# Optimization experiments

Measured on AMD Instinct MI355X. Metric: run time of the kernel, lower is better.

The kernel has to match this reference:

```python
import jax, jax.numpy as jnp
import numpy as np

HEADS = 8
DIM_HEAD = 32
EPS = 1e-5


def _rel_index(h, w):
    # matches Attention._generate_relative_index (static, computed on host)
    coords = np.stack(np.meshgrid(np.arange(h), np.arange(w), indexing='ij')).reshape(2, -1)
    rel = coords[:, :, None] - coords[:, None, :]  # [2, n, n]
    rel[0] += h - 1
    rel[1] += w - 1
    rel[0] *= 2 * w - 1
    idx = rel.sum(0).reshape(-1)
    # torch.clamp(relative_index, 0, max_index) -- indices are already in range here
    return jnp.asarray(np.clip(idx, 0, (2 * h - 1) * (2 * w - 1) - 1))


def _layernorm(x, g, b):
    m = jnp.mean(x, axis=-1, keepdims=True)
    v = jnp.var(x, axis=-1, keepdims=True)
    return (x - m) * jax.lax.rsqrt(v + EPS) * g + b


def setup_inputs() -> dict:
    key = jax.random.key(0)
    ks = jax.random.split(key, 6)
    B, C, H, W = 64, 384, 16, 16
    inner = HEADS * DIM_HEAD  # 256
    hid = 4 * C               # 1536
    def nrm(k, shape, s=0.02):
        return jax.random.normal(k, shape, jnp.float32) * s
    return {
        'x': jax.random.normal(ks[0], (B, C, H, W), jnp.float32),
        'ln1_g': jnp.ones((C,), jnp.float32),
        'ln1_b': jnp.zeros((C,), jnp.float32),
        'w_qkv': nrm(ks[1], (C, 3 * inner)),
        'bias_table': nrm(ks[2], ((2 * H - 1) * (2 * W - 1), HEADS)),
        'w_out': nrm(ks[3], (inner, C)),
        'b_out': jnp.zeros((C,), jnp.float32),
        'ln2_g': jnp.ones((C,), jnp.float32),
        'ln2_b': jnp.zeros((C,), jnp.float32),
        'w_ff1': nrm(ks[4], (C, hid)),
        'b_ff1': jnp.zeros((hid,), jnp.float32),
        'w_ff2': nrm(ks[5], (hid, C)),
        'b_ff2': jnp.zeros((C,), jnp.float32),
    }


def reference(x, ln1_g, ln1_b, w_qkv, bias_table, w_out, b_out,
              ln2_g, ln2_b, w_ff1, b_ff1, w_ff2, b_ff2):
    B, C, H, W = x.shape
    n = H * W
    t = x.reshape(B, C, n).transpose(0, 2, 1)  # [B, n, C]

    # --- attention branch (PreNorm(LayerNorm) -> Attention) ---
    a = _layernorm(t, ln1_g, ln1_b)
    qkv = a @ w_qkv  # [B, n, 3*inner]
    q, k, v = jnp.split(qkv, 3, axis=-1)
    def split_heads(z):
        return z.reshape(B, n, HEADS, DIM_HEAD).transpose(0, 2, 1, 3)  # [B, h, n, d]
    q, k, v = split_heads(q), split_heads(k), split_heads(v)
    dots = jnp.einsum('bhid,bhjd->bhij', q, k) * (DIM_HEAD ** -0.5)
    idx = _rel_index(H, W)  # [n*n]
    rel_bias = bias_table[idx].reshape(n, n, HEADS).transpose(2, 0, 1)[None]  # [1, h, n, n]
    attn = jax.nn.softmax(dots + rel_bias, axis=-1)
    o = jnp.einsum('bhij,bhjd->bhid', attn, v)
    o = o.transpose(0, 2, 1, 3).reshape(B, n, HEADS * DIM_HEAD)
    attn_out = o @ w_out + b_out  # to_out Linear (dropout=0)

    # --- feedforward branch (PreNorm(LayerNorm) -> FFN) ---
    f = _layernorm(t, ln2_g, ln2_b)
    f = jax.nn.gelu(f @ w_ff1 + b_ff1, approximate=False) @ w_ff2 + b_ff2

    y = t + attn_out + f  # x_adjusted + attn_out + ff_out
    return y.transpose(0, 2, 1).reshape(B, C, H, W)
```

## Files before the change

kernel.cpp:

```cpp
#include <hip/hip_runtime.h>

typedef __bf16 bf16;
typedef __bf16 bf16x8 __attribute__((ext_vector_type(8)));
typedef float f32x4 __attribute__((ext_vector_type(4)));

__device__ __forceinline__ void gll16(const void* g, void* l) {
    __builtin_amdgcn_global_load_lds((const __attribute__((address_space(1))) void*)g,
                                     (__attribute__((address_space(3))) void*)l, 16, 0, 0);
}

#define WBAR(N) asm volatile("s_waitcnt vmcnt(" #N ")\n\ts_barrier" ::: "memory")

__device__ __forceinline__ float gelu_f(float v) {
    float x2 = v * v;
    float sn = v * fmaf(-0.0713540072f, x2, -1.5957691216f);
    float e  = __expf(sn);
    return v * __builtin_amdgcn_rcpf(1.0f + e);
}

__launch_bounds__(256)
__global__ void prep_kernel(const float* __restrict__ wqkv, const float* __restrict__ wout,
                            const float* __restrict__ wff1, const float* __restrict__ wff2,
                            bf16* __restrict__ wqkvT, bf16* __restrict__ woutT,
                            bf16* __restrict__ wff1T, bf16* __restrict__ wff2T,
                            const float* __restrict__ x,
                            const float* __restrict__ g1, const float* __restrict__ b1,
                            const float* __restrict__ g2, const float* __restrict__ b2,
                            bf16* __restrict__ a, bf16* __restrict__ f) {
    __shared__ __align__(16) float smem[12672 + 512 + 64];
    const int tid = threadIdx.x;
    int g = blockIdx.x;
    if (g < 1536) {
        float (*tl)[33] = (float (*)[33])smem;
        const float* in; bf16* out; int R, Cc, bx, by;
        if (g < 288)       { in = wqkv; out = wqkvT; R = 384;  Cc = 768;  bx = g % 24; by = g / 24; }
        else if (g < 384)  { g -= 288; in = wout; out = woutT; R = 256;  Cc = 384;  bx = g % 12; by = g / 12; }
        else if (g < 960)  { g -= 384; in = wff1; out = wff1T; R = 384;  Cc = 1536; bx = g % 48; by = g / 48; }
        else               { g -= 960; in = wff2; out = wff2T; R = 1536; Cc = 384;  bx = g % 12; by = g / 12; }
        const int c0 = bx * 32, r0 = by * 32;
        const int cl = tid & 31, r8 = tid >> 5;
#pragma unroll
        for (int k = 0; k < 4; k++) {
            int r = k * 8 + r8;
            tl[r][cl] = in[(size_t)(r0 + r) * Cc + c0 + cl];
        }
        __syncthreads();
#pragma unroll
        for (int k = 0; k < 4; k++) {
            int cc = k * 8 + r8;
            out[(size_t)(c0 + cc) * R + r0 + cl] = (bf16)tl[cl][cc];
        }
        return;
    }
    g -= 1536;
    float (*tile)[33] = (float (*)[33])smem;
    float (*S)[32]  = (float (*)[32])(smem + 12672);
    float (*SS)[32] = (float (*)[32])(smem + 12928);
    float* Mn = smem + 13184;
    float* Rs = smem + 13216;
    const int bb = g >> 3;
    const int i0 = (g & 7) * 32;
    {
        const int i_l = tid & 31, c_l = tid >> 5;
        const size_t base = (size_t)bb * 384 * 256 + i0 + i_l;
#pragma unroll 6
        for (int c = c_l; c < 384; c += 8)
            tile[c][i_l] = x[base + (size_t)c * 256];
    }
    __syncthreads();
    {
        const int i_s = tid & 31, p = tid >> 5;
        float s = 0.f, ss = 0.f;
#pragma unroll 6
        for (int j = 0; j < 48; j++) {
            float v = tile[p * 48 + j][i_s];
            s += v; ss += v * v;
        }
        S[p][i_s] = s; SS[p][i_s] = ss;
    }
    __syncthreads();
    if (tid < 32) {
        float t1 = 0.f, t2 = 0.f;
#pragma unroll
        for (int p = 0; p < 8; p++) { t1 += S[p][tid]; t2 += SS[p][tid]; }
        float mean = t1 * (1.0f / 384.0f);
        float var  = t2 * (1.0f / 384.0f) - mean * mean;
        Mn[tid] = mean;
        Rs[tid] = rsqrtf(var + 1e-5f);
    }
    __syncthreads();
    const int lane = tid & 63, w = tid >> 6;
#pragma unroll
    for (int rr = 0; rr < 8; rr++) {
        const int i = w * 8 + rr;
        const float mean = Mn[i], rstd = Rs[i];
        const size_t orow = ((size_t)bb * 256 + i0 + i) * 384;
#pragma unroll
        for (int pass = 0; pass < 6; pass++) {
            const int c = pass * 64 + lane;
            float nh = (tile[c][i] - mean) * rstd;
            a[orow + c] = (bf16)(nh * g1[c] + b1[c]);
            f[orow + c] = (bf16)(nh * g2[c] + b2[c]);
        }
    }
}

#define STAGEW(buf, kb)                                                     \
    {                                                                       \
        bf16* sA = lds + (buf) * 12288;                                     \
        bf16* sB = sA + 4096;                                               \
        gll16(Abase + (size_t)rS * K + (kb) + ksw, sA + tid * 8);           \
        gll16(Abase + (size_t)(rS + 64) * K + (kb) + ksw, sA + (tid + 256) * 8); \
        gll16(Bbase + (size_t)rS * K + (kb) + ksw, sB + tid * 8);           \
        gll16(Bbase + (size_t)(rS + 64) * K + (kb) + ksw, sB + (tid + 256) * 8); \
        gll16(Bbase + (size_t)(rS + 128) * K + (kb) + ksw, sB + (tid + 512) * 8); \
        gll16(Bbase + (size_t)(rS + 192) * K + (kb) + ksw, sB + (tid + 768) * 8); \
    }
#define COMPUTEW(buf)                                                       \
    {                                                                       \
        const bf16* sA = lds + (buf) * 12288;                               \
        const bf16* sB = sA + 4096;                                         \
        bf16x8 af[4], bfr[8];                                               \
        _Pragma("unroll") for (int i = 0; i < 4; i++)                       \
            af[i] = *(const bf16x8*)(sA + (wm + i * 16 + l16) * 32 + rsw);  \
        _Pragma("unroll") for (int j = 0; j < 8; j++)                       \
            bfr[j] = *(const bf16x8*)(sB + (wn + j * 16 + l16) * 32 + rsw); \
        _Pragma("unroll") for (int i = 0; i < 4; i++)                       \
            _Pragma("unroll") for (int j = 0; j < 8; j++)                   \
                acc[i][j] = __builtin_amdgcn_mfma_f32_16x16x32_bf16(af[i], bfr[j], acc[i][j], 0, 0, 0); \
    }

template <int EPI>
__launch_bounds__(256)
__global__ void gemm_w(const bf16* __restrict__ A, const bf16* __restrict__ Bt,
                       const float* __restrict__ bias, bf16* __restrict__ C,
                       int M, int N, int K, int nx) {
    __shared__ __align__(16) bf16 lds[36864];
    const int tid = threadIdx.x;
    const int g = blockIdx.x;
    const int x_ = (g >> 3) % nx;
    const int y_ = (g & 7) + 8 * (g / (8 * nx));
    const int m0 = y_ * 128, n0 = x_ * 256;
    const int lane = tid & 63, w = tid >> 6;
    const int l16 = lane & 15, quad = lane >> 4;
    const int wm = (w & 1) * 64, wn = (w >> 1) * 128;
    f32x4 acc[4][8];
    { f32x4 z = {0.f, 0.f, 0.f, 0.f};
#pragma unroll
      for (int i = 0; i < 4; i++)
#pragma unroll
          for (int j = 0; j < 8; j++) acc[i][j] = z; }
    const int rS = tid >> 2;
    const int ksw = (((tid & 3) ^ ((tid >> 3) & 3)) * 8);
    const int rsw = ((quad ^ ((l16 >> 1) & 3)) * 8);
    const bf16* Abase = A + (size_t)m0 * K;
    const bf16* Bbase = Bt + (size_t)n0 * K;

    STAGEW(0, 0);
    STAGEW(1, 32);
    const int nt = K >> 5;
    int t = 0;
    for (; t < nt - 2; ++t) {
        WBAR(6);
        STAGEW((t + 2) % 3, (t + 2) * 32);
        COMPUTEW(t % 3);
    }
    WBAR(6); COMPUTEW(t % 3); ++t;
    WBAR(0); COMPUTEW(t % 3);
    __syncthreads();

#pragma unroll
    for (int j = 0; j < 8; j++) {
        const int col = wn + j * 16 + l16;
        float bv = 0.f;
        if (EPI >= 1) bv = bias[n0 + col];
#pragma unroll
        for (int i = 0; i < 4; i++) {
            const int row0 = wm + i * 16 + quad * 4;
#pragma unroll
            for (int r = 0; r < 4; r++) {
                float v = acc[i][j][r] + bv;
                if (EPI == 2) v = gelu_f(v);
                lds[(row0 + r) * 256 + col] = (bf16)v;
            }
        }
    }
    __syncthreads();
#pragma unroll
    for (int it = 0; it < 16; it++) {
        const int ch = tid + it * 256;
        const int row = ch >> 5, cc = (ch & 31) * 8;
        *(bf16x8*)(C + (size_t)(m0 + row) * N + n0 + cc) = *(const bf16x8*)(lds + row * 256 + cc);
    }
}

#define COMPUTE128(buf)                                                     \
    {                                                                       \
        const bf16* sA = lds + (buf) * 8192;                                \
        const bf16* sB = sA + 4096;                                         \
        bf16x8 af[4], bfr[4];                                               \
        _Pragma("unroll") for (int i = 0; i < 4; i++)                       \
            af[i] = *(const bf16x8*)(sA + (wm + i * 16 + l16) * 32 + rsw);  \
        _Pragma("unroll") for (int j = 0; j < 4; j++)                       \
            bfr[j] = *(const bf16x8*)(sB + (wn + j * 16 + l16) * 32 + rsw); \
        _Pragma("unroll") for (int i = 0; i < 4; i++)                       \
            _Pragma("unroll") for (int j = 0; j < 4; j++)                   \
                acc[i][j] = __builtin_amdgcn_mfma_f32_16x16x32_bf16(af[i], bfr[j], acc[i][j], 0, 0, 0); \
    }

__launch_bounds__(256)
__global__ void fin_dual(const bf16* __restrict__ Af, const bf16* __restrict__ Bf,
                         const bf16* __restrict__ Ao, const bf16* __restrict__ Bo,
                         const float* __restrict__ bff2, const float* __restrict__ bout,
                         const float* __restrict__ xres, float* __restrict__ out, int nx) {
    __shared__ __align__(16) bf16 lds[24576];
    const int tid = threadIdx.x;
    const int g = blockIdx.x;
    const int x_ = (g >> 3) % nx;
    const int y_ = (g & 7) + 8 * (g / (8 * nx));
    const int m0 = y_ * 128, n0 = x_ * 128;
    const int lane = tid & 63, w = tid >> 6;
    const int l16 = lane & 15, quad = lane >> 4;
    const int wm = (w & 1) * 64, wn = (w >> 1) * 64;
    f32x4 acc[4][4];
    { f32x4 z = {0.f, 0.f, 0.f, 0.f};
#pragma unroll
      for (int i = 0; i < 4; i++)
#pragma unroll
          for (int j = 0; j < 4; j++) acc[i][j] = z; }
    const int c0 = tid, c1 = tid + 256;
    const int r0 = c0 >> 2, r1 = c1 >> 2;
    const int ksw = (((tid & 3) ^ ((tid >> 3) & 3)) * 8);
    const int rsw = ((quad ^ ((l16 >> 1) & 3)) * 8);
    const bf16* A1 = Af + (size_t)m0 * 1536;
    const bf16* B1 = Bf + (size_t)n0 * 1536;
    const bf16* A2 = Ao + (size_t)m0 * 256;
    const bf16* B2 = Bo + (size_t)n0 * 256;

#define STGD(buf, s)                                                                \
    {   bf16* sA = lds + (buf) * 8192;                                              \
        bf16* sB = sA + 4096;                                                       \
        if ((s) < 48) {                                                             \
            const int kb = (s) * 32;                                                \
            gll16(A1 + (size_t)r0 * 1536 + kb + ksw, sA + c0 * 8);                  \
            gll16(A1 + (size_t)r1 * 1536 + kb + ksw, sA + c1 * 8);                  \
            gll16(B1 + (size_t)r0 * 1536 + kb + ksw, sB + c0 * 8);                  \
            gll16(B1 + (size_t)r1 * 1536 + kb + ksw, sB + c1 * 8);                  \
        } else {                                                                    \
            const int kb = ((s) - 48) * 32;                                         \
            gll16(A2 + (size_t)r0 * 256 + kb + ksw, sA + c0 * 8);                   \
            gll16(A2 + (size_t)r1 * 256 + kb + ksw, sA + c1 * 8);                   \
            gll16(B2 + (size_t)r0 * 256 + kb + ksw, sB + c0 * 8);                   \
            gll16(B2 + (size_t)r1 * 256 + kb + ksw, sB + c1 * 8);                   \
        } }

    STGD(0, 0); STGD(1, 1);
    int s = 0;
    for (; s < 54; ++s) {
        WBAR(4);
        STGD((s + 2) % 3, s + 2);
        COMPUTE128(s % 3);
    }
    WBAR(4); COMPUTE128(s % 3); ++s;
    WBAR(0); COMPUTE128(s % 3);
    __syncthreads();
#undef STGD

#pragma unroll
    for (int j = 0; j < 4; j++) {
        const int col = wn + j * 16 + l16;
        const float bv = bff2[n0 + col] + bout[n0 + col];
#pragma unroll
        for (int i = 0; i < 4; i++) {
            const int row0 = wm + i * 16 + quad * 4;
#pragma unroll
            for (int r = 0; r < 4; r++)
                lds[col * 132 + row0 + r] = (bf16)(acc[i][j][r] + bv);
        }
    }
    __syncthreads();
    const int b = m0 >> 8, ib = m0 & 255;
#pragma unroll
    for (int it = 0; it < 8; it++) {
        const int ch = tid + it * 256;
        const int cl = ch >> 4, ic = (ch & 15) * 8;
        const size_t base = (size_t)(b * 384 + n0 + cl) * 256 + ib + ic;
        bf16x8 ff = *(const bf16x8*)(lds + cl * 132 + ic);
        const f32x4* xr = (const f32x4*)(xres + base);
        f32x4 o0, o1;
#pragma unroll
        for (int e = 0; e < 4; e++) o0[e] = xr[0][e] + (float)ff[e];
#pragma unroll
        for (int e = 0; e < 4; e++) o1[e] = xr[1][e] + (float)ff[e + 4];
        ((f32x4*)(out + base))[0] = o0;
        ((f32x4*)(out + base))[1] = o1;
    }
}

__launch_bounds__(256)
__global__ void attn_kernel(const bf16* __restrict__ qkv,
                            const float* __restrict__ btab,
                            bf16* __restrict__ o) {
    __shared__ float sbias[961];
    __shared__ __align__(16) bf16 sK[256 * 32];
    __shared__ __align__(16) bf16 sVt[32][264];
    __shared__ __align__(16) bf16 sP[4][16][264];
    const int tid = threadIdx.x;
    const int g = blockIdx.x;
    const int h  = (g >> 3) & 7;
    const int bb = (g & 7) + 8 * (g >> 6);
    const int lane = tid & 63, w = tid >> 6;
    const int l16 = lane & 15, quad = lane >> 4;
    const int rsw = ((quad ^ ((l16 >> 1) & 3)) * 8);
    const size_t qkvb = (size_t)bb * 256 * 768;
    const bf16* Qbase = qkv + qkvb + h * 32;
    const bf16* Kbase = qkv + qkvb + 256 + h * 32;
    const bf16* Vbase = qkv + qkvb + 512 + h * 32;

    for (int e = tid; e < 961; e += 256) sbias[e] = btab[e * 8 + h];
#pragma unroll
    for (int it = 0; it < 4; it++) {
        const int ch = it * 256 + tid;
        const int row = ch >> 2;
        const int d8 = (((ch & 3) ^ ((ch >> 3) & 3)) * 8);
        gll16(Kbase + (size_t)row * 768 + d8, sK + ch * 8);
    }
#pragma unroll
    for (int it = 0; it < 4; it++) {
        const int ch = it * 256 + tid;
        const int k = ch >> 2, d8 = (ch & 3) * 8;
        bf16x8 vv = *(const bf16x8*)(Vbase + (size_t)k * 768 + d8);
#pragma unroll
        for (int j = 0; j < 8; j++)
            sVt[d8 + j][k] = vv[j];
    }
    __syncthreads();

    f32x4 zero = {0.f, 0.f, 0.f, 0.f};
    for (int qc = 0; qc < 4; qc++) {
        const int qbase = qc * 64 + w * 16;
        bf16x8 qf = *(const bf16x8*)(Qbase + (size_t)(qbase + l16) * 768 + quad * 8);
        f32x4 s[16];
#pragma unroll
        for (int kt = 0; kt < 16; kt++) {
            bf16x8 kf = *(const bf16x8*)(sK + (kt * 16 + l16) * 32 + rsw);
            s[kt] = __builtin_amdgcn_mfma_f32_16x16x32_bf16(qf, kf, zero, 0, 0, 0);
        }
        const int qi0 = qbase + quad * 4;
        float mx[4] = {-1e30f, -1e30f, -1e30f, -1e30f};
#pragma unroll
        for (int kt = 0; kt < 16; kt++) {
            const int j = kt * 16 + l16;
            const int yj = j >> 4, xj = j & 15;
#pragma unroll
            for (int r = 0; r < 4; r++) {
                const int q = qi0 + r;
                const int tix = ((q >> 4) - yj + 15) * 31 + ((q & 15) - xj + 15);
                float v = s[kt][r] * 0.17677669529663687f + sbias[tix];
                s[kt][r] = v;
                mx[r] = fmaxf(mx[r], v);
            }
        }
#pragma unroll
        for (int r = 0; r < 4; r++)
            for (int msk = 1; msk < 16; msk <<= 1)
                mx[r] = fmaxf(mx[r], __shfl_xor(mx[r], msk, 64));
        float sum[4] = {0.f, 0.f, 0.f, 0.f};
#pragma unroll
        for (int kt = 0; kt < 16; kt++)
#pragma unroll
            for (int r = 0; r < 4; r++) {
                float e = __expf(s[kt][r] - mx[r]);
                s[kt][r] = e;
                sum[r] += e;
            }
#pragma unroll
        for (int r = 0; r < 4; r++) {
            for (int msk = 1; msk < 16; msk <<= 1)
                sum[r] += __shfl_xor(sum[r], msk, 64);
            sum[r] = 1.0f / sum[r];
        }
#pragma unroll
        for (int kt = 0; kt < 16; kt++)
#pragma unroll
            for (int r = 0; r < 4; r++)
                sP[w][quad * 4 + r][kt * 16 + l16] = (bf16)(s[kt][r] * sum[r]);
        f32x4 oacc[2];
        oacc[0] = zero; oacc[1] = zero;
#pragma unroll
        for (int ks = 0; ks < 8; ks++) {
            bf16x8 pf = *(const bf16x8*)(&sP[w][l16][ks * 32 + quad * 8]);
#pragma unroll
            for (int dt = 0; dt < 2; dt++) {
                bf16x8 vf = *(const bf16x8*)(&sVt[dt * 16 + l16][ks * 32 + quad * 8]);
                oacc[dt] = __builtin_amdgcn_mfma_f32_16x16x32_bf16(pf, vf, oacc[dt], 0, 0, 0);
            }
        }
#pragma unroll
        for (int dt = 0; dt < 2; dt++)
#pragma unroll
            for (int r = 0; r < 4; r++)
                o[(size_t)(bb * 256 + qbase + quad * 4 + r) * 256 + h * 32 + dt * 16 + l16] = (bf16)oacc[dt][r];
    }
}

extern "C" void kernel_launch(void* const* d_in, const int* in_sizes, int n_in,
                              void* d_out, int out_size, void* d_ws, size_t ws_size,
                              hipStream_t stream) {
    const float* x    = (const float*)d_in[0];
    const float* g1   = (const float*)d_in[1];
    const float* b1   = (const float*)d_in[2];
    const float* wqkv = (const float*)d_in[3];
    const float* btab = (const float*)d_in[4];
    const float* wout = (const float*)d_in[5];
    const float* bout = (const float*)d_in[6];
    const float* g2   = (const float*)d_in[7];
    const float* b2   = (const float*)d_in[8];
    const float* wff1 = (const float*)d_in[9];
    const float* bff1 = (const float*)d_in[10];
    const float* wff2 = (const float*)d_in[11];
    const float* bff2 = (const float*)d_in[12];
    float* out = (float*)d_out;

    bf16* ws = (bf16*)d_ws;
    const size_t NA = 6291456;
    bf16* wqkvT   = ws;
    bf16* woutT   = wqkvT + 294912;
    bf16* wff1T   = woutT + 98304;
    bf16* wff2T   = wff1T + 589824;
    bf16* f_buf   = ws + 1572864;
    bf16* a_buf   = f_buf + NA;
    bf16* qkv_buf = a_buf + NA;
    bf16* o_buf   = qkv_buf + 12582912;
    bf16* ffh_buf = o_buf + 4194304;

    dim3 b256(256);
    prep_kernel<<<2048, b256, 0, stream>>>(wqkv, wout, wff1, wff2, wqkvT, woutT, wff1T, wff2T,
                                           x, g1, b1, g2, b2, a_buf, f_buf);
    gemm_w<0><<<3 * 128, b256, 0, stream>>>(a_buf, wqkvT, nullptr, qkv_buf, 16384, 768, 384, 3);
    attn_kernel<<<512, b256, 0, stream>>>(qkv_buf, btab, o_buf);
    gemm_w<2><<<6 * 128, b256, 0, stream>>>(f_buf, wff1T, bff1, ffh_buf, 16384, 1536, 384, 6);
    fin_dual<<<3 * 128, b256, 0, stream>>>(ffh_buf, wff2T, o_buf, woutT, bff2, bout, x, out, 3);
}
```

Before: 232.6 us.

## Enlarge QKV and FF1 GEMM tiles to 256x256 with 512 threads, fold q-scale

```diff
diff --git a/kernel.cpp b/kernel.cpp
--- a/kernel.cpp
+++ b/kernel.cpp
@@ -105,21 +105,19 @@
     }
 }
 
-#define STAGEW(buf, kb)                                                     \
+#define STAGE256(buf, kb)                                                   \
     {                                                                       \
-        bf16* sA = lds + (buf) * 12288;                                     \
-        bf16* sB = sA + 4096;                                               \
+        bf16* sA = lds + (buf) * 16384;                                     \
+        bf16* sB = sA + 8192;                                               \
         gll16(Abase + (size_t)rS * K + (kb) + ksw, sA + tid * 8);           \
-        gll16(Abase + (size_t)(rS + 64) * K + (kb) + ksw, sA + (tid + 256) * 8); \
+        gll16(Abase + (size_t)(rS + 128) * K + (kb) + ksw, sA + (tid + 512) * 8); \
         gll16(Bbase + (size_t)rS * K + (kb) + ksw, sB + tid * 8);           \
-        gll16(Bbase + (size_t)(rS + 64) * K + (kb) + ksw, sB + (tid + 256) * 8); \
         gll16(Bbase + (size_t)(rS + 128) * K + (kb) + ksw, sB + (tid + 512) * 8); \
-        gll16(Bbase + (size_t)(rS + 192) * K + (kb) + ksw, sB + (tid + 768) * 8); \
-    }
-#define COMPUTEW(buf)                                                       \
+    }
+#define COMPUTE256(buf)                                                     \
     {                                                                       \
-        const bf16* sA = lds + (buf) * 12288;                               \
-        const bf16* sB = sA + 4096;                                         \
+        const bf16* sA = lds + (buf) * 16384;                               \
+        const bf16* sB = sA + 8192;                                         \
         bf16x8 af[4], bfr[8];                                               \
         _Pragma("unroll") for (int i = 0; i < 4; i++)                       \
             af[i] = *(const bf16x8*)(sA + (wm + i * 16 + l16) * 32 + rsw);  \
@@ -131,19 +129,19 @@
     }
 
 template <int EPI>
-__launch_bounds__(256)
-__global__ void gemm_w(const bf16* __restrict__ A, const bf16* __restrict__ Bt,
-                       const float* __restrict__ bias, bf16* __restrict__ C,
-                       int M, int N, int K, int nx) {
-    __shared__ __align__(16) bf16 lds[36864];
+__launch_bounds__(512)
+__global__ void gemm256(const bf16* __restrict__ A, const bf16* __restrict__ Bt,
+                        const float* __restrict__ bias, bf16* __restrict__ C,
+                        int M, int N, int K, int nx) {
+    __shared__ __align__(16) bf16 lds[49152];
     const int tid = threadIdx.x;
     const int g = blockIdx.x;
     const int x_ = (g >> 3) % nx;
     const int y_ = (g & 7) + 8 * (g / (8 * nx));
-    const int m0 = y_ * 128, n0 = x_ * 256;
+    const int m0 = y_ * 256, n0 = x_ * 256;
     const int lane = tid & 63, w = tid >> 6;
     const int l16 = lane & 15, quad = lane >> 4;
-    const int wm = (w & 1) * 64, wn = (w >> 1) * 128;
+    const int wm = (w & 3) * 64, wn = (w >> 2) * 128;
     f32x4 acc[4][8];
     { f32x4 z = {0.f, 0.f, 0.f, 0.f};
 #pragma unroll
@@ -156,41 +154,51 @@
     const bf16* Abase = A + (size_t)m0 * K;
     const bf16* Bbase = Bt + (size_t)n0 * K;
 
-    STAGEW(0, 0);
-    STAGEW(1, 32);
+    STAGE256(0, 0);
+    STAGE256(1, 32);
     const int nt = K >> 5;
     int t = 0;
     for (; t < nt - 2; ++t) {
-        WBAR(6);
-        STAGEW((t + 2) % 3, (t + 2) * 32);
-        COMPUTEW(t % 3);
-    }
-    WBAR(6); COMPUTEW(t % 3); ++t;
-    WBAR(0); COMPUTEW(t % 3);
-    __syncthreads();
-
-#pragma unroll
-    for (int j = 0; j < 8; j++) {
-        const int col = wn + j * 16 + l16;
-        float bv = 0.f;
-        if (EPI >= 1) bv = bias[n0 + col];
-#pragma unroll
-        for (int i = 0; i < 4; i++) {
-            const int row0 = wm + i * 16 + quad * 4;
-#pragma unroll
-            for (int r = 0; r < 4; r++) {
-                float v = acc[i][j][r] + bv;
-                if (EPI == 2) v = gelu_f(v);
-                lds[(row0 + r) * 256 + col] = (bf16)v;
+        WBAR(4);
+        STAGE256((t + 2) % 3, (t + 2) * 32);
+        COMPUTE256(t % 3);
+    }
+    WBAR(4); COMPUTE256(t % 3); ++t;
+    WBAR(0); COMPUTE256(t % 3);
+    __syncthreads();
+
+    const float qsc = (EPI == 3 && n0 < 256) ? 0.17677669529663687f : 1.0f;
+#pragma unroll
+    for (int pass = 0; pass < 2; pass++) {
+        if (((w & 3) >> 1) == pass) {
+            const int rbase = wm & 127;
+#pragma unroll
+            for (int j = 0; j < 8; j++) {
+                const int col = wn + j * 16 + l16;
+                float bv = 0.f;
+                if (EPI == 2) bv = bias[n0 + col];
+#pragma unroll
+                for (int i = 0; i < 4; i++) {
+                    const int row0 = rbase + i * 16 + quad * 4;
+#pragma unroll
+                    for (int r = 0; r < 4; r++) {
+                        float v = acc[i][j][r];
+                        if (EPI == 3) v *= qsc;
+                        if (EPI == 2) v = gelu_f(v + bv);
+                        lds[(row0 + r) * 256 + col] = (bf16)v;
+                    }
+                }
             }
         }
-    }
-    __syncthreads();
-#pragma unroll
-    for (int it = 0; it < 16; it++) {
-        const int ch = tid + it * 256;
-        const int row = ch >> 5, cc = (ch & 31) * 8;
-        *(bf16x8*)(C + (size_t)(m0 + row) * N + n0 + cc) = *(const bf16x8*)(lds + row * 256 + cc);
+        __syncthreads();
+#pragma unroll
+        for (int it = 0; it < 8; it++) {
+            const int ch = tid + it * 512;
+            const int row = ch >> 5, cc = (ch & 31) * 8;
+            *(bf16x8*)(C + (size_t)(m0 + pass * 128 + row) * N + n0 + cc) =
+                *(const bf16x8*)(lds + row * 256 + cc);
+        }
+        __syncthreads();
     }
 }
 
@@ -356,7 +364,7 @@
             for (int r = 0; r < 4; r++) {
                 const int q = qi0 + r;
                 const int tix = ((q >> 4) - yj + 15) * 31 + ((q & 15) - xj + 15);
-                float v = s[kt][r] * 0.17677669529663687f + sbias[tix];
+                float v = s[kt][r] + sbias[tix];
                 s[kt][r] = v;
                 mx[r] = fmaxf(mx[r], v);
             }
@@ -435,10 +443,11 @@
     bf16* ffh_buf = o_buf + 4194304;
 
     dim3 b256(256);
+    dim3 b512(512);
     prep_kernel<<<2048, b256, 0, stream>>>(wqkv, wout, wff1, wff2, wqkvT, woutT, wff1T, wff2T,
                                            x, g1, b1, g2, b2, a_buf, f_buf);
-    gemm_w<0><<<3 * 128, b256, 0, stream>>>(a_buf, wqkvT, nullptr, qkv_buf, 16384, 768, 384, 3);
+    gemm256<3><<<192, b512, 0, stream>>>(a_buf, wqkvT, nullptr, qkv_buf, 16384, 768, 384, 3);
     attn_kernel<<<512, b256, 0, stream>>>(qkv_buf, btab, o_buf);
-    gemm_w<2><<<6 * 128, b256, 0, stream>>>(f_buf, wff1T, bff1, ffh_buf, 16384, 1536, 384, 6);
+    gemm256<2><<<384, b512, 0, stream>>>(f_buf, wff1T, bff1, ffh_buf, 16384, 1536, 384, 6);
     fin_dual<<<3 * 128, b256, 0, stream>>>(ffh_buf, wff2T, o_buf, woutT, bff2, bout, x, out, 3);
 }
```

After: 238.3 us. 1.02x slower.
